# Kernel tuning notes

Hardware: AMD Instinct MI355X
Metric: run time of the kernel (lower is better)

The kernel has to match this reference:

```python
import jax, jax.numpy as jnp
import numpy as np

B, S, E, D = 32, 2048, 1024, 1024


def setup_inputs() -> dict:
    key = jax.random.key(0)
    k0, k1, k2, k3, k4 = jax.random.split(key, 5)
    scale_e = 1.0 / np.sqrt(E)
    scale_d = 1.0 / np.sqrt(D)
    return {
        "hidden": jax.random.normal(k0, (B, D), dtype=jnp.float32),
        "encoder_outputs": jax.random.normal(k1, (S, B, E), dtype=jnp.float32),
        "We": jax.random.normal(k2, (D, E), dtype=jnp.float32) * scale_e,
        "Wd": jax.random.normal(k3, (D, D), dtype=jnp.float32) * scale_d,
        "v": jax.random.normal(k4, (D,), dtype=jnp.float32) * scale_d,
    }


def reference(hidden, encoder_outputs, We, Wd, v):
    # encoder projection: [S,B,E] x [D,E] -> [B,S,D] (batch-first for the add)
    enc_proj = jnp.einsum("sbe,de->bsd", encoder_outputs, We)
    # decoder projection broadcast over src positions: [B,1,D]
    dec_proj = (hidden @ Wd.T)[:, None, :]
    energy = jnp.tanh(enc_proj + dec_proj)          # [B,S,D]
    scores = jnp.einsum("bsd,d->bs", energy, v)     # v-layer, squeeze(-1)
    attention_weights = jax.nn.softmax(scores, axis=1)  # softmax over src_len
    # weighted sum of encoder outputs: bmm([B,1,S],[B,S,E]) -> [B,E]
    context = jnp.einsum("bs,sbe->be", attention_weights, encoder_outputs)
    return context, attention_weights
```

## Files before the change

### kernel.cpp

```cpp
#include <hip/hip_runtime.h>
#include <cmath>
#include <cstdint>

constexpr int B_ = 32;
constexpr int S_ = 2048;
constexpr int E_ = 1024;
constexpr int D_ = 1024;
constexpr int K_ = E_;
constexpr int M_ = S_ * B_;
constexpr int SC_ = 32;
constexpr int NP_ = 16;

typedef float f32x4 __attribute__((ext_vector_type(4)));
typedef __bf16 bf16x8 __attribute__((ext_vector_type(8)));

__device__ __forceinline__ float fast_tanh(float x) {
    float e = __builtin_amdgcn_exp2f(x * 2.88539008177793f);
    return 1.f - 2.f * __builtin_amdgcn_rcpf(e + 1.f);
}

__device__ __forceinline__ uint16_t f2bf(float f) {
    uint32_t u = __float_as_uint(f);
    u += 0x7FFFu + ((u >> 16) & 1u);
    return (uint16_t)(u >> 16);
}

constexpr int ENC_N8 = M_ * K_ / 8;
constexpr int WE_N8  = D_ * K_ / 8;
constexpr int CVT_BLOCKS = (ENC_N8 + WE_N8) / 256;

__global__ __launch_bounds__(256) void convert_kernel(
    const float* __restrict__ enc, uint16_t* __restrict__ encb,
    const float* __restrict__ We,  uint16_t* __restrict__ Web)
{
    int tid = blockIdx.x * 256 + threadIdx.x;
    const float* src;
    uint16_t* dst;
    int i8;
    if (tid < ENC_N8) { src = enc; dst = encb; i8 = tid; }
    else              { src = We;  dst = Web;  i8 = tid - ENC_N8; }
    const float4* s4 = reinterpret_cast<const float4*>(src) + i8 * 2;
    float4 a = s4[0], b = s4[1];
    uint4 o;
    o.x = (uint32_t)f2bf(a.x) | ((uint32_t)f2bf(a.y) << 16);
    o.y = (uint32_t)f2bf(a.z) | ((uint32_t)f2bf(a.w) << 16);
    o.z = (uint32_t)f2bf(b.x) | ((uint32_t)f2bf(b.y) << 16);
    o.w = (uint32_t)f2bf(b.z) | ((uint32_t)f2bf(b.w) << 16);
    reinterpret_cast<uint4*>(dst)[i8] = o;
}

__global__ __launch_bounds__(256) void dec_proj_wave_kernel(
    const float* __restrict__ hidden, const float* __restrict__ Wd,
    float* __restrict__ dec)
{
    const int o = blockIdx.x * 4 + (threadIdx.x >> 6);
    const int lane = threadIdx.x & 63;
    const int b = o >> 10;
    const int d = o & (D_ - 1);
    const float4* h4 = reinterpret_cast<const float4*>(hidden + (size_t)b * D_);
    const float4* w4 = reinterpret_cast<const float4*>(Wd + (size_t)d * D_);
    float acc = 0.f;
#pragma unroll
    for (int p = 0; p < 4; ++p) {
        float4 h = h4[lane + p * 64], w = w4[lane + p * 64];
        acc += h.x * w.x + h.y * w.y + h.z * w.z + h.w * w.w;
    }
#pragma unroll
    for (int off = 32; off > 0; off >>= 1) acc += __shfl_xor(acc, off);
    if (lane == 0) dec[o] = acc;
}

constexpr int TM = 128, TN = 128;

__global__ __launch_bounds__(256) void score_mfma_kernel(
    const uint16_t* __restrict__ A,
    const uint16_t* __restrict__ Bw,
    const float* __restrict__ dec,
    const float* __restrict__ v,
    float* __restrict__ spart)
{
    __shared__ __align__(16) uint16_t As[2][TM * 32];
    __shared__ __align__(16) uint16_t Bs[2][TN * 32];

    const int p    = blockIdx.x;
    const int xcd  = p & 7;
    const int slot = p >> 3;
    const int nb   = slot & 7;
    const int mb   = xcd + 8 * (slot >> 3);
    const int m0 = mb * TM;
    const int n0 = nb * TN;

    const int t    = threadIdx.x;
    const int wave = t >> 6;
    const int lane = t & 63;
    const int wm   = (wave & 1) * 64;
    const int wn   = (wave >> 1) * 64;
    const int q    = lane >> 4;
    const int r16  = lane & 15;

    const int srow = lane >> 2;
    const int scol = (lane & 3) * 8;

    f32x4 acc[4][4] = {};

    for (int k0 = 0; k0 < K_; k0 += 64) {
        __syncthreads();
#pragma unroll
        for (int h = 0; h < 2; ++h) {
            const int kk = k0 + h * 32;
#pragma unroll
            for (int i = 0; i < 2; ++i) {
                const int c = wave * 2 + i;
                const uint16_t* ga = A + (size_t)(m0 + c * 16 + srow) * K_ + kk + scol;
                __builtin_amdgcn_global_load_lds(
                    (const __attribute__((address_space(1))) uint32_t*)ga,
                    (__attribute__((address_space(3))) uint32_t*)(As[h] + c * 512),
                    16, 0, 0);
                const uint16_t* gb = Bw + (size_t)(n0 + c * 16 + srow) * K_ + kk + scol;
                __builtin_amdgcn_global_load_lds(
                    (const __attribute__((address_space(1))) uint32_t*)gb,
                    (__attribute__((address_space(3))) uint32_t*)(Bs[h] + c * 512),
                    16, 0, 0);
            }
        }
        __syncthreads();

#pragma unroll
        for (int h = 0; h < 2; ++h) {
            bf16x8 af[4], bf[4];
#pragma unroll
            for (int i = 0; i < 4; ++i) {
                af[i] = __builtin_bit_cast(bf16x8,
                    *reinterpret_cast<const int4*>(As[h] + (wm + i * 16 + r16) * 32 + q * 8));
                bf[i] = __builtin_bit_cast(bf16x8,
                    *reinterpret_cast<const int4*>(Bs[h] + (wn + i * 16 + r16) * 32 + q * 8));
            }
#pragma unroll
            for (int i = 0; i < 4; ++i)
#pragma unroll
                for (int j = 0; j < 4; ++j)
                    acc[i][j] = __builtin_amdgcn_mfma_f32_16x16x32_bf16(
                        af[i], bf[j], acc[i][j], 0, 0, 0);
        }
    }

    float vj[4];
#pragma unroll
    for (int j = 0; j < 4; ++j) vj[j] = v[n0 + wn + j * 16 + r16];

    float* plane = spart + (size_t)(nb * 2 + (wn >> 6)) * M_;

#pragma unroll
    for (int i = 0; i < 4; ++i) {
#pragma unroll
        for (int r = 0; r < 4; ++r) {
            const int m = m0 + wm + i * 16 + q * 4 + r;
            const int b = m & (B_ - 1);
            float pv = 0.f;
#pragma unroll
            for (int j = 0; j < 4; ++j) {
                const int n = n0 + wn + j * 16 + r16;
                pv += vj[j] * fast_tanh(acc[i][j][r] + dec[b * D_ + n]);
            }
            pv += __shfl_xor(pv, 1);
            pv += __shfl_xor(pv, 2);
            pv += __shfl_xor(pv, 4);
            pv += __shfl_xor(pv, 8);
            if (r16 == 0) plane[b * S_ + (m >> 5)] = pv;
        }
    }
}

__global__ __launch_bounds__(256) void softmax16_kernel(
    const float* __restrict__ spart,
    float* __restrict__ attn)
{
    const int b = blockIdx.x;
    const int t = threadIdx.x;
    __shared__ float sm[256];

    const float4* base = reinterpret_cast<const float4*>(spart + (size_t)b * S_);
    constexpr int PSTRIDE = M_ / 4;
    float4 v0 = {0, 0, 0, 0}, v1 = {0, 0, 0, 0};
#pragma unroll
    for (int p = 0; p < NP_; ++p) {
        float4 a = base[(size_t)p * PSTRIDE + t];
        float4 c = base[(size_t)p * PSTRIDE + t + 256];
        v0.x += a.x; v0.y += a.y; v0.z += a.z; v0.w += a.w;
        v1.x += c.x; v1.y += c.y; v1.z += c.z; v1.w += c.w;
    }

    float lmax = fmaxf(fmaxf(fmaxf(v0.x, v0.y), fmaxf(v0.z, v0.w)),
                       fmaxf(fmaxf(v1.x, v1.y), fmaxf(v1.z, v1.w)));
    sm[t] = lmax; __syncthreads();
    for (int off = 128; off > 0; off >>= 1) {
        if (t < off) sm[t] = fmaxf(sm[t], sm[t + off]);
        __syncthreads();
    }
    const float mx = sm[0];
    __syncthreads();

    v0.x = __builtin_amdgcn_exp2f((v0.x - mx) * 1.44269504f);
    v0.y = __builtin_amdgcn_exp2f((v0.y - mx) * 1.44269504f);
    v0.z = __builtin_amdgcn_exp2f((v0.z - mx) * 1.44269504f);
    v0.w = __builtin_amdgcn_exp2f((v0.w - mx) * 1.44269504f);
    v1.x = __builtin_amdgcn_exp2f((v1.x - mx) * 1.44269504f);
    v1.y = __builtin_amdgcn_exp2f((v1.y - mx) * 1.44269504f);
    v1.z = __builtin_amdgcn_exp2f((v1.z - mx) * 1.44269504f);
    v1.w = __builtin_amdgcn_exp2f((v1.w - mx) * 1.44269504f);

    float lsum = v0.x + v0.y + v0.z + v0.w + v1.x + v1.y + v1.z + v1.w;
    sm[t] = lsum; __syncthreads();
    for (int off = 128; off > 0; off >>= 1) {
        if (t < off) sm[t] += sm[t + off];
        __syncthreads();
    }
    const float inv = 1.f / sm[0];
    float4* op = reinterpret_cast<float4*>(attn + (size_t)b * S_);
    v0.x *= inv; v0.y *= inv; v0.z *= inv; v0.w *= inv;
    v1.x *= inv; v1.y *= inv; v1.z *= inv; v1.w *= inv;
    op[t] = v0; op[t + 256] = v1;
}

__global__ __launch_bounds__(256) void context_part_kernel(
    const uint16_t* __restrict__ encb, const float* __restrict__ attn,
    float* __restrict__ part)
{
    const int b  = blockIdx.x & (B_ - 1);
    const int sc = blockIdx.x >> 5;
    const int e0 = threadIdx.x * 4;
    constexpr int SLEN = S_ / SC_;

    float a0 = 0.f, a1 = 0.f, a2 = 0.f, a3 = 0.f;
    const int s0 = sc * SLEN;
#pragma unroll 2
    for (int s = s0; s < s0 + SLEN; ++s) {
        const float w = attn[b * S_ + s];
        uint2 u = *reinterpret_cast<const uint2*>(
            encb + ((size_t)s * B_ + b) * E_ + e0);
        a0 += w * __uint_as_float((u.x & 0xFFFFu) << 16);
        a1 += w * __uint_as_float(u.x & 0xFFFF0000u);
        a2 += w * __uint_as_float((u.y & 0xFFFFu) << 16);
        a3 += w * __uint_as_float(u.y & 0xFFFF0000u);
    }
    float4 o = {a0, a1, a2, a3};
    *reinterpret_cast<float4*>(part + ((size_t)sc * B_ + b) * E_ + e0) = o;
}

__global__ __launch_bounds__(256) void context_reduce_kernel(
    const float* __restrict__ part, float* __restrict__ ctx)
{
    const int i = blockIdx.x * 256 + threadIdx.x;
    float acc = 0.f;
#pragma unroll
    for (int sc = 0; sc < SC_; ++sc) acc += part[(size_t)sc * B_ * E_ + i];
    ctx[i] = acc;
}

constexpr int BM = 64, BN = 64, BK = 16;

__global__ __launch_bounds__(256) void score_gemm_kernel(
    const float* __restrict__ enc, const float* __restrict__ We,
    const float* __restrict__ dec, const float* __restrict__ v,
    float* __restrict__ scores)
{
    __shared__ float As[BM][BK + 1];
    __shared__ float Bs[BN][BK + 1];
    __shared__ float red[BM][17];
    const int m0 = blockIdx.x * BM;
    const int n0 = blockIdx.y * BN;
    const int t  = threadIdx.x;
    const int tx = t & 15;
    const int ty = t >> 4;
    const int lrow = t >> 2;
    const int lcol = (t & 3) * 4;
    float acc[4][4] = {};
    for (int k0 = 0; k0 < E_; k0 += BK) {
        float4 a = *reinterpret_cast<const float4*>(enc + (size_t)(m0 + lrow) * E_ + k0 + lcol);
        float4 w = *reinterpret_cast<const float4*>(We + (size_t)(n0 + lrow) * E_ + k0 + lcol);
        As[lrow][lcol + 0] = a.x; As[lrow][lcol + 1] = a.y;
        As[lrow][lcol + 2] = a.z; As[lrow][lcol + 3] = a.w;
        Bs[lrow][lcol + 0] = w.x; Bs[lrow][lcol + 1] = w.y;
        Bs[lrow][lcol + 2] = w.z; Bs[lrow][lcol + 3] = w.w;
        __syncthreads();
#pragma unroll
        for (int kk = 0; kk < BK; ++kk) {
            float av[4], bw[4];
#pragma unroll
            for (int i = 0; i < 4; ++i) av[i] = As[ty * 4 + i][kk];
#pragma unroll
            for (int j = 0; j < 4; ++j) bw[j] = Bs[tx * 4 + j][kk];
#pragma unroll
            for (int i = 0; i < 4; ++i)
#pragma unroll
                for (int j = 0; j < 4; ++j)
                    acc[i][j] += av[i] * bw[j];
        }
        __syncthreads();
    }
    float pp[4];
#pragma unroll
    for (int i = 0; i < 4; ++i) {
        int m = m0 + ty * 4 + i;
        int b = m & (B_ - 1);
        float s = 0.f;
#pragma unroll
        for (int j = 0; j < 4; ++j) {
            int n = n0 + tx * 4 + j;
            s += v[n] * tanhf(acc[i][j] + dec[b * D_ + n]);
        }
        pp[i] = s;
    }
#pragma unroll
    for (int i = 0; i < 4; ++i) red[ty * 4 + i][tx] = pp[i];
    __syncthreads();
    if (t < BM) {
        float s = 0.f;
#pragma unroll
        for (int j = 0; j < 16; ++j) s += red[t][j];
        atomicAdd(&scores[m0 + t], s);
    }
}

__global__ __launch_bounds__(256) void softmax_kernel(
    const float* __restrict__ scores, float* __restrict__ attn)
{
    const int b = blockIdx.x;
    const int t = threadIdx.x;
    __shared__ float sm[256];
    float vals[8];
    float lmax = -INFINITY;
#pragma unroll
    for (int i = 0; i < 8; ++i) {
        int s = t + i * 256;
        vals[i] = scores[s * B_ + b];
        lmax = fmaxf(lmax, vals[i]);
    }
    sm[t] = lmax; __syncthreads();
    for (int off = 128; off > 0; off >>= 1) {
        if (t < off) sm[t] = fmaxf(sm[t], sm[t + off]);
        __syncthreads();
    }
    const float mx = sm[0];
    __syncthreads();
    float lsum = 0.f;
#pragma unroll
    for (int i = 0; i < 8; ++i) {
        vals[i] = expf(vals[i] - mx);
        lsum += vals[i];
    }
    sm[t] = lsum; __syncthreads();
    for (int off = 128; off > 0; off >>= 1) {
        if (t < off) sm[t] += sm[t + off];
        __syncthreads();
    }
    const float inv = 1.f / sm[0];
#pragma unroll
    for (int i = 0; i < 8; ++i)
        attn[b * S_ + t + i * 256] = vals[i] * inv;
}

__global__ __launch_bounds__(256) void context_kernel(
    const float* __restrict__ enc, const float* __restrict__ attn,
    float* __restrict__ ctx)
{
    const int e0 = (blockIdx.x & 3) * 256;
    const int b  = (blockIdx.x >> 2) & (B_ - 1);
    const int sc = blockIdx.x >> 7;
    const int e  = e0 + threadIdx.x;
    float acc = 0.f;
    const int s_end = sc * 256 + 256;
    for (int s = sc * 256; s < s_end; ++s)
        acc += attn[b * S_ + s] * enc[((size_t)s * B_ + b) * E_ + e];
    atomicAdd(&ctx[b * E_ + e], acc);
}

extern "C" void kernel_launch(void* const* d_in, const int* in_sizes, int n_in,
                              void* d_out, int out_size, void* d_ws, size_t ws_size,
                              hipStream_t stream) {
    const float* hidden = (const float*)d_in[0];
    const float* enc    = (const float*)d_in[1];
    const float* We     = (const float*)d_in[2];
    const float* Wd     = (const float*)d_in[3];
    const float* v      = (const float*)d_in[4];

    float* ctx  = (float*)d_out;
    float* attn = (float*)d_out + B_ * E_;

    float*    dec   = (float*)d_ws;
    float*    spart = dec + B_ * D_;
    uint16_t* Web   = (uint16_t*)(spart + (size_t)NP_ * M_);
    uint16_t* encb  = Web + (size_t)D_ * K_;

    const size_t need = (size_t)B_ * D_ * 4 + (size_t)NP_ * M_ * 4
                      + ((size_t)D_ * K_ + (size_t)M_ * K_) * 2;
    const bool fast = ws_size >= need;

    if (fast) {
        convert_kernel<<<CVT_BLOCKS, 256, 0, stream>>>(enc, encb, We, Web);
        dec_proj_wave_kernel<<<(B_ * D_) / 4, 256, 0, stream>>>(hidden, Wd, dec);

        score_mfma_kernel<<<(M_ / TM) * (D_ / TN), 256, 0, stream>>>(
            encb, Web, dec, v, spart);

        softmax16_kernel<<<B_, 256, 0, stream>>>(spart, attn);
        context_part_kernel<<<SC_ * B_, 256, 0, stream>>>(encb, attn, spart);
        context_reduce_kernel<<<(B_ * E_) / 256, 256, 0, stream>>>(spart, ctx);
    } else {
        float* scores = spart;
        hipMemsetAsync(scores, 0, (size_t)M_ * sizeof(float), stream);
        hipMemsetAsync(ctx, 0, (size_t)B_ * E_ * sizeof(float), stream);
        dec_proj_wave_kernel<<<(B_ * D_) / 4, 256, 0, stream>>>(hidden, Wd, dec);
        dim3 g2(M_ / BM, D_ / BN);
        score_gemm_kernel<<<g2, 256, 0, stream>>>(enc, We, dec, v, scores);
        softmax_kernel<<<B_, 256, 0, stream>>>(scores, attn);
        context_kernel<<<B_ * 4 * 8, 256, 0, stream>>>(enc, attn, ctx);
    }
}
```

Before: 600.2 us.

## Fuse conversion and decoder projection into one prep kernel; preload epilogue operands

Merges the bf16 conversion kernel and the decoder-projection kernel into a single launch split by block index, and switches the large fp32 reads to nontemporal loads. In the MFMA score kernel, the global-to-LDS source pointers are precomputed and advanced by increments, and v and the needed dec values are loaded into registers before the K loop instead of inside the epilogue. This is meant to save one launch, reduce address arithmetic, and hide epilogue load latency. The cost is higher register pressure in the GEMM kernel.

```diff
diff --git a/kernel.cpp b/kernel.cpp
--- a/kernel.cpp
+++ b/kernel.cpp
@@ -12,6 +12,7 @@
 constexpr int NP_ = 16;
 
 typedef float f32x4 __attribute__((ext_vector_type(4)));
+typedef float fvec4 __attribute__((ext_vector_type(4)));
 typedef __bf16 bf16x8 __attribute__((ext_vector_type(8)));
 
 __device__ __forceinline__ float fast_tanh(float x) {
@@ -28,46 +29,48 @@
 constexpr int ENC_N8 = M_ * K_ / 8;
 constexpr int WE_N8  = D_ * K_ / 8;
 constexpr int CVT_BLOCKS = (ENC_N8 + WE_N8) / 256;
-
-__global__ __launch_bounds__(256) void convert_kernel(
+constexpr int DEC_BLOCKS = (B_ * D_) / 4;
+
+__global__ __launch_bounds__(256) void prep_kernel(
     const float* __restrict__ enc, uint16_t* __restrict__ encb,
-    const float* __restrict__ We,  uint16_t* __restrict__ Web)
-{
-    int tid = blockIdx.x * 256 + threadIdx.x;
-    const float* src;
-    uint16_t* dst;
-    int i8;
-    if (tid < ENC_N8) { src = enc; dst = encb; i8 = tid; }
-    else              { src = We;  dst = Web;  i8 = tid - ENC_N8; }
-    const float4* s4 = reinterpret_cast<const float4*>(src) + i8 * 2;
-    float4 a = s4[0], b = s4[1];
-    uint4 o;
-    o.x = (uint32_t)f2bf(a.x) | ((uint32_t)f2bf(a.y) << 16);
-    o.y = (uint32_t)f2bf(a.z) | ((uint32_t)f2bf(a.w) << 16);
-    o.z = (uint32_t)f2bf(b.x) | ((uint32_t)f2bf(b.y) << 16);
-    o.w = (uint32_t)f2bf(b.z) | ((uint32_t)f2bf(b.w) << 16);
-    reinterpret_cast<uint4*>(dst)[i8] = o;
-}
-
-__global__ __launch_bounds__(256) void dec_proj_wave_kernel(
+    const float* __restrict__ We,  uint16_t* __restrict__ Web,
     const float* __restrict__ hidden, const float* __restrict__ Wd,
     float* __restrict__ dec)
 {
-    const int o = blockIdx.x * 4 + (threadIdx.x >> 6);
-    const int lane = threadIdx.x & 63;
-    const int b = o >> 10;
-    const int d = o & (D_ - 1);
-    const float4* h4 = reinterpret_cast<const float4*>(hidden + (size_t)b * D_);
-    const float4* w4 = reinterpret_cast<const float4*>(Wd + (size_t)d * D_);
-    float acc = 0.f;
-#pragma unroll
-    for (int p = 0; p < 4; ++p) {
-        float4 h = h4[lane + p * 64], w = w4[lane + p * 64];
-        acc += h.x * w.x + h.y * w.y + h.z * w.z + h.w * w.w;
-    }
-#pragma unroll
-    for (int off = 32; off > 0; off >>= 1) acc += __shfl_xor(acc, off);
-    if (lane == 0) dec[o] = acc;
+    const int bid = blockIdx.x;
+    if (bid < CVT_BLOCKS) {
+        int tid = bid * 256 + threadIdx.x;
+        const float* src;
+        uint16_t* dst;
+        int i8;
+        if (tid < ENC_N8) { src = enc; dst = encb; i8 = tid; }
+        else              { src = We;  dst = Web;  i8 = tid - ENC_N8; }
+        const fvec4* s4 = reinterpret_cast<const fvec4*>(src) + (size_t)i8 * 2;
+        fvec4 a = __builtin_nontemporal_load(s4);
+        fvec4 b = __builtin_nontemporal_load(s4 + 1);
+        uint4 o;
+        o.x = (uint32_t)f2bf(a.x) | ((uint32_t)f2bf(a.y) << 16);
+        o.y = (uint32_t)f2bf(a.z) | ((uint32_t)f2bf(a.w) << 16);
+        o.z = (uint32_t)f2bf(b.x) | ((uint32_t)f2bf(b.y) << 16);
+        o.w = (uint32_t)f2bf(b.z) | ((uint32_t)f2bf(b.w) << 16);
+        reinterpret_cast<uint4*>(dst)[i8] = o;
+    } else {
+        const int o = (bid - CVT_BLOCKS) * 4 + (threadIdx.x >> 6);
+        const int lane = threadIdx.x & 63;
+        const int b = o >> 10;
+        const int d = o & (D_ - 1);
+        const float4* h4 = reinterpret_cast<const float4*>(hidden + (size_t)b * D_);
+        const float4* w4 = reinterpret_cast<const float4*>(Wd + (size_t)d * D_);
+        float acc = 0.f;
+#pragma unroll
+        for (int p = 0; p < 4; ++p) {
+            float4 h = h4[lane + p * 64], w = w4[lane + p * 64];
+            acc += h.x * w.x + h.y * w.y + h.z * w.z + h.w * w.w;
+        }
+#pragma unroll
+        for (int off = 32; off > 0; off >>= 1) acc += __shfl_xor(acc, off);
+        if (lane == 0) dec[o] = acc;
+    }
 }
 
 constexpr int TM = 128, TN = 128;
@@ -101,28 +104,54 @@
     const int srow = lane >> 2;
     const int scol = (lane & 3) * 8;
 
+    const int c0 = wave * 2, c1 = wave * 2 + 1;
+    const uint16_t* ga00 = A + (size_t)(m0 + c0 * 16 + srow) * K_ + scol;
+    const uint16_t* ga01 = ga00 + 32;
+    const uint16_t* ga10 = A + (size_t)(m0 + c1 * 16 + srow) * K_ + scol;
+    const uint16_t* ga11 = ga10 + 32;
+    const uint16_t* gb00 = Bw + (size_t)(n0 + c0 * 16 + srow) * K_ + scol;
+    const uint16_t* gb01 = gb00 + 32;
+    const uint16_t* gb10 = Bw + (size_t)(n0 + c1 * 16 + srow) * K_ + scol;
+    const uint16_t* gb11 = gb10 + 32;
+    typedef __attribute__((address_space(3))) uint32_t lds_u32;
+    typedef const __attribute__((address_space(1))) uint32_t g_u32;
+    lds_u32* dA00 = (lds_u32*)(As[0] + c0 * 512);
+    lds_u32* dA01 = (lds_u32*)(As[1] + c0 * 512);
+    lds_u32* dA10 = (lds_u32*)(As[0] + c1 * 512);
+    lds_u32* dA11 = (lds_u32*)(As[1] + c1 * 512);
+    lds_u32* dB00 = (lds_u32*)(Bs[0] + c0 * 512);
+    lds_u32* dB01 = (lds_u32*)(Bs[1] + c0 * 512);
+    lds_u32* dB10 = (lds_u32*)(Bs[0] + c1 * 512);
+    lds_u32* dB11 = (lds_u32*)(Bs[1] + c1 * 512);
+
+    float vj[4];
+#pragma unroll
+    for (int j = 0; j < 4; ++j) vj[j] = v[n0 + wn + j * 16 + r16];
+    float dec_r[2][4][4];
+#pragma unroll
+    for (int i01 = 0; i01 < 2; ++i01)
+#pragma unroll
+        for (int r = 0; r < 4; ++r) {
+            const int b = i01 * 16 + q * 4 + r;
+#pragma unroll
+            for (int j = 0; j < 4; ++j)
+                dec_r[i01][r][j] = dec[b * D_ + n0 + wn + j * 16 + r16];
+        }
+
     f32x4 acc[4][4] = {};
 
-    for (int k0 = 0; k0 < K_; k0 += 64) {
-        __syncthreads();
-#pragma unroll
-        for (int h = 0; h < 2; ++h) {
-            const int kk = k0 + h * 32;
-#pragma unroll
-            for (int i = 0; i < 2; ++i) {
-                const int c = wave * 2 + i;
-                const uint16_t* ga = A + (size_t)(m0 + c * 16 + srow) * K_ + kk + scol;
-                __builtin_amdgcn_global_load_lds(
-                    (const __attribute__((address_space(1))) uint32_t*)ga,
-                    (__attribute__((address_space(3))) uint32_t*)(As[h] + c * 512),
-                    16, 0, 0);
-                const uint16_t* gb = Bw + (size_t)(n0 + c * 16 + srow) * K_ + kk + scol;
-                __builtin_amdgcn_global_load_lds(
-                    (const __attribute__((address_space(1))) uint32_t*)gb,
-                    (__attribute__((address_space(3))) uint32_t*)(Bs[h] + c * 512),
-                    16, 0, 0);
-            }
-        }
+    for (int it = 0; it < K_ / 64; ++it) {
+        __syncthreads();
+        __builtin_amdgcn_global_load_lds((g_u32*)ga00, dA00, 16, 0, 0);
+        __builtin_amdgcn_global_load_lds((g_u32*)ga01, dA01, 16, 0, 0);
+        __builtin_amdgcn_global_load_lds((g_u32*)ga10, dA10, 16, 0, 0);
+        __builtin_amdgcn_global_load_lds((g_u32*)ga11, dA11, 16, 0, 0);
+        __builtin_amdgcn_global_load_lds((g_u32*)gb00, dB00, 16, 0, 0);
+        __builtin_amdgcn_global_load_lds((g_u32*)gb01, dB01, 16, 0, 0);
+        __builtin_amdgcn_global_load_lds((g_u32*)gb10, dB10, 16, 0, 0);
+        __builtin_amdgcn_global_load_lds((g_u32*)gb11, dB11, 16, 0, 0);
+        ga00 += 64; ga01 += 64; ga10 += 64; ga11 += 64;
+        gb00 += 64; gb01 += 64; gb10 += 64; gb11 += 64;
         __syncthreads();
 
 #pragma unroll
@@ -144,10 +173,6 @@
         }
     }
 
-    float vj[4];
-#pragma unroll
-    for (int j = 0; j < 4; ++j) vj[j] = v[n0 + wn + j * 16 + r16];
-
     float* plane = spart + (size_t)(nb * 2 + (wn >> 6)) * M_;
 
 #pragma unroll
@@ -155,13 +180,11 @@
 #pragma unroll
         for (int r = 0; r < 4; ++r) {
             const int m = m0 + wm + i * 16 + q * 4 + r;
-            const int b = m & (B_ - 1);
+            const int b = (i & 1) * 16 + q * 4 + r;
             float pv = 0.f;
 #pragma unroll
-            for (int j = 0; j < 4; ++j) {
-                const int n = n0 + wn + j * 16 + r16;
-                pv += vj[j] * fast_tanh(acc[i][j][r] + dec[b * D_ + n]);
-            }
+            for (int j = 0; j < 4; ++j)
+                pv += vj[j] * fast_tanh(acc[i][j][r] + dec_r[i & 1][r][j]);
             pv += __shfl_xor(pv, 1);
             pv += __shfl_xor(pv, 2);
             pv += __shfl_xor(pv, 4);
@@ -258,6 +281,27 @@
 }
 
 constexpr int BM = 64, BN = 64, BK = 16;
+
+__global__ __launch_bounds__(256) void dec_proj_wave_kernel(
+    const float* __restrict__ hidden, const float* __restrict__ Wd,
+    float* __restrict__ dec)
+{
+    const int o = blockIdx.x * 4 + (threadIdx.x >> 6);
+    const int lane = threadIdx.x & 63;
+    const int b = o >> 10;
+    const int d = o & (D_ - 1);
+    const float4* h4 = reinterpret_cast<const float4*>(hidden + (size_t)b * D_);
+    const float4* w4 = reinterpret_cast<const float4*>(Wd + (size_t)d * D_);
+    float acc = 0.f;
+#pragma unroll
+    for (int p = 0; p < 4; ++p) {
+        float4 h = h4[lane + p * 64], w = w4[lane + p * 64];
+        acc += h.x * w.x + h.y * w.y + h.z * w.z + h.w * w.w;
+    }
+#pragma unroll
+    for (int off = 32; off > 0; off >>= 1) acc += __shfl_xor(acc, off);
+    if (lane == 0) dec[o] = acc;
+}
 
 __global__ __launch_bounds__(256) void score_gemm_kernel(
     const float* __restrict__ enc, const float* __restrict__ We,
@@ -397,8 +441,8 @@
     const bool fast = ws_size >= need;
 
     if (fast) {
-        convert_kernel<<<CVT_BLOCKS, 256, 0, stream>>>(enc, encb, We, Web);
-        dec_proj_wave_kernel<<<(B_ * D_) / 4, 256, 0, stream>>>(hidden, Wd, dec);
+        prep_kernel<<<CVT_BLOCKS + DEC_BLOCKS, 256, 0, stream>>>(
+            enc, encb, We, Web, hidden, Wd, dec);
 
         score_mfma_kernel<<<(M_ / TM) * (D_ / TN), 256, 0, stream>>>(
             encb, Web, dec, v, spart);
```

Result: faster. 561.4 us (-6.5%).
